# Kernel tuning notes

Hardware: AMD Instinct MI355X
Metric: run time of the kernel (lower is better)

The kernel has to match this reference:

```python
import jax, jax.numpy as jnp
import numpy as np

N_NODES = 50000
N_EDGES = 800000
F_IN = 128
F_OUT = 128
N_REL = 4
BN_EPS = 1e-5


def setup_inputs() -> dict:
    key = jax.random.key(0)
    ks = jax.random.split(key, 12)
    s = 1.0 / np.sqrt(F_IN)
    inp = {
        "x": jax.random.normal(ks[0], (N_NODES, F_IN), dtype=jnp.float32),
        "edge_index": jax.random.randint(ks[1], (2, N_EDGES), 0, N_NODES, dtype=jnp.int64),
        "edge_type": jax.random.randint(ks[2], (N_EDGES,), 0, N_REL, dtype=jnp.int64),
        # self-loop linear
        "W_self": jax.random.uniform(ks[3], (F_IN, F_OUT), jnp.float32, -s, s),
        "b_self": jax.random.uniform(ks[4], (F_OUT,), jnp.float32, -s, s),
        # per-relation GIN MLP: Linear -> BatchNorm1d -> ReLU -> Linear (stacked over relations)
        "W1": jax.random.uniform(ks[5], (N_REL, F_IN, F_OUT), jnp.float32, -s, s),
        "b1": jax.random.uniform(ks[6], (N_REL, F_OUT), jnp.float32, -s, s),
        "gamma": jnp.ones((N_REL, F_OUT), jnp.float32),
        "beta": jnp.zeros((N_REL, F_OUT), jnp.float32),
        "W2": jax.random.uniform(ks[7], (N_REL, F_OUT, F_OUT), jnp.float32, -1.0 / np.sqrt(F_OUT), 1.0 / np.sqrt(F_OUT)),
        "b2": jax.random.uniform(ks[8], (N_REL, F_OUT), jnp.float32, -1.0 / np.sqrt(F_OUT), 1.0 / np.sqrt(F_OUT)),
    }
    return inp


def reference(x, edge_index, edge_type, W_self, b_self, W1, b1, gamma, beta, W2, b2):
    N = x.shape[0]
    R = W1.shape[0]
    src, dst = edge_index[0], edge_index[1]
    # single fused scatter-add over (relation, dst): segment id = rel*N + dst
    msg = x[src]                                        # [E, F_in]
    seg = edge_type * N + dst                           # [E]
    agg = jax.ops.segment_sum(msg, seg, num_segments=R * N).reshape(R, N, -1)  # [R, N, F_in]
    # GIN with eps=0: h = x + sum of neighbor messages, per relation
    h = x[None, :, :] + agg                             # [R, N, F_in]
    # MLP: Linear -> BatchNorm1d (batch stats over nodes) -> ReLU -> Linear
    h = jnp.einsum('rnf,rfg->rng', h, W1) + b1[:, None, :]
    mean = jnp.mean(h, axis=1, keepdims=True)
    var = jnp.var(h, axis=1, keepdims=True)
    h = (h - mean) * jax.lax.rsqrt(var + BN_EPS) * gamma[:, None, :] + beta[:, None, :]
    h = jax.nn.relu(h)
    out_rel = jnp.einsum('rng,rgk->rnk', h, W2) + b2[:, None, :]  # [R, N, F_out]
    return x @ W_self + b_self + jnp.sum(out_rel, axis=0)
```

## Files before the change

### kernel.cpp

```cpp
#include <hip/hip_runtime.h>

#define NN 50000
#define NE 800000
#define F 128
#define NREL 4
#define RN (NREL * NN)
#define NB 196
#define BN_EPS 1e-5f
#define TILE 128
#define NT1 391
#define LDW 136

typedef __attribute__((ext_vector_type(8))) short short8;
typedef __attribute__((ext_vector_type(4))) float floatx4;

__device__ __forceinline__ ushort f2bf(float f) {
    union { float f; unsigned u; } v; v.f = f;
    unsigned r = v.u + 0x7fffu + ((v.u >> 16) & 1u);
    return (ushort)(r >> 16);
}
__device__ __forceinline__ float bf2f(ushort h) {
    union { unsigned u; float f; } v; v.u = ((unsigned)h) << 16;
    return v.f;
}
__device__ __forceinline__ float ubf(unsigned bits) {
    union { unsigned u; float f; } v; v.u = bits; return v.f;
}
__device__ __forceinline__ unsigned pk2(float a, float b) {
    return (unsigned)f2bf(a) | ((unsigned)f2bf(b) << 16);
}
__device__ __forceinline__ void acc_u4(float* acc, uint4 v) {
    acc[0] += ubf(v.x << 16); acc[1] += ubf(v.x & 0xffff0000u);
    acc[2] += ubf(v.y << 16); acc[3] += ubf(v.y & 0xffff0000u);
    acc[4] += ubf(v.z << 16); acc[5] += ubf(v.z & 0xffff0000u);
    acc[6] += ubf(v.w << 16); acc[7] += ubf(v.w & 0xffff0000u);
}

__global__ __launch_bounds__(256) void xb_kernel(
    const float* __restrict__ x, ushort* __restrict__ xb)
{
    int i = blockIdx.x * 256 + threadIdx.x;
    float4 v = *(const float4*)(x + (size_t)i * 4);
    uint2 u;
    u.x = pk2(v.x, v.y);
    u.y = pk2(v.z, v.w);
    *(uint2*)(xb + (size_t)i * 4) = u;
}

__global__ __launch_bounds__(256) void hist_kernel(
    const int* __restrict__ ei, const int* __restrict__ et, int* __restrict__ counts)
{
    int e = blockIdx.x * 256 + threadIdx.x;
    if (e >= NE) return;
    atomicAdd(&counts[et[e] * NN + ei[NE + e]], 1);
}

__global__ __launch_bounds__(256) void scan1_kernel(
    const int* __restrict__ counts, int* __restrict__ rowptr, int* __restrict__ bsum)
{
    __shared__ int wsum[4];
    const int tid = threadIdx.x;
    const int base = blockIdx.x * 1024 + tid * 4;
    int c[4];
    #pragma unroll
    for (int j = 0; j < 4; j++) c[j] = (base + j < RN) ? counts[base + j] : 0;
    int tsum = c[0] + c[1] + c[2] + c[3];
    const int lane = tid & 63, wv = tid >> 6;
    int s = tsum;
    #pragma unroll
    for (int d = 1; d < 64; d <<= 1) { int t = __shfl_up(s, d); if (lane >= d) s += t; }
    if (lane == 63) wsum[wv] = s;
    __syncthreads();
    int wave_off = 0;
    #pragma unroll
    for (int w = 0; w < 4; w++) if (w < wv) wave_off += wsum[w];
    int run = wave_off + s - tsum;
    #pragma unroll
    for (int j = 0; j < 4; j++) {
        if (base + j < RN) rowptr[base + j] = run;
        run += c[j];
    }
    if (tid == 0) bsum[blockIdx.x] = wsum[0] + wsum[1] + wsum[2] + wsum[3];
}

__global__ __launch_bounds__(256) void scan2_kernel(
    const int* __restrict__ bsum, int* __restrict__ boff, int* __restrict__ rowptr)
{
    __shared__ int wsum[4];
    const int tid = threadIdx.x;
    int v = (tid < NB) ? bsum[tid] : 0;
    const int lane = tid & 63, wv = tid >> 6;
    int s = v;
    #pragma unroll
    for (int d = 1; d < 64; d <<= 1) { int t = __shfl_up(s, d); if (lane >= d) s += t; }
    if (lane == 63) wsum[wv] = s;
    __syncthreads();
    int wave_off = 0;
    #pragma unroll
    for (int w = 0; w < 4; w++) if (w < wv) wave_off += wsum[w];
    if (tid < NB) boff[tid] = wave_off + s - v;
    if (tid == 0) rowptr[RN] = wsum[0] + wsum[1] + wsum[2] + wsum[3];
}

__global__ __launch_bounds__(256) void scan3_kernel(
    int* __restrict__ rowptr, const int* __restrict__ boff, int* __restrict__ cursor)
{
    const int base = blockIdx.x * 1024 + threadIdx.x * 4;
    const int off = boff[blockIdx.x];
    #pragma unroll
    for (int j = 0; j < 4; j++) {
        int idx = base + j;
        if (idx < RN) { int v = rowptr[idx] + off; rowptr[idx] = v; cursor[idx] = v; }
    }
}

__global__ __launch_bounds__(256) void reorder_kernel(
    const int* __restrict__ ei, const int* __restrict__ et,
    int* __restrict__ cursor, int* __restrict__ sorted_src)
{
    int e = blockIdx.x * 256 + threadIdx.x;
    if (e >= NE) return;
    int key = et[e] * NN + ei[NE + e];
    int pos = atomicAdd(&cursor[key], 1);
    sorted_src[pos] = ei[e];
}

__global__ __launch_bounds__(256) void gather_kernel(
    const ushort* __restrict__ xb, const int* __restrict__ rowptr,
    const int* __restrict__ sorted_src, ushort* __restrict__ hbuf)
{
    const int t = blockIdx.x * 256 + threadIdx.x;
    const int row = t >> 4;
    const int lane = t & 15;
    const int n = row % NN;

    const uint4* xv = (const uint4*)xb;
    float acc[8];
    {
        uint4 v = xv[n * 16 + lane];
        acc[0] = ubf(v.x << 16); acc[1] = ubf(v.x & 0xffff0000u);
        acc[2] = ubf(v.y << 16); acc[3] = ubf(v.y & 0xffff0000u);
        acc[4] = ubf(v.z << 16); acc[5] = ubf(v.z & 0xffff0000u);
        acc[6] = ubf(v.w << 16); acc[7] = ubf(v.w & 0xffff0000u);
    }
    int e = rowptr[row];
    const int e1 = rowptr[row + 1];
    for (; e + 4 <= e1; e += 4) {
        int s0 = sorted_src[e], s1 = sorted_src[e + 1];
        int s2 = sorted_src[e + 2], s3 = sorted_src[e + 3];
        uint4 a = xv[s0 * 16 + lane];
        uint4 b = xv[s1 * 16 + lane];
        uint4 c = xv[s2 * 16 + lane];
        uint4 d = xv[s3 * 16 + lane];
        acc_u4(acc, a); acc_u4(acc, b); acc_u4(acc, c); acc_u4(acc, d);
    }
    for (; e < e1; ++e) {
        int s0 = sorted_src[e];
        acc_u4(acc, xv[s0 * 16 + lane]);
    }
    uint4 o;
    o.x = pk2(acc[0], acc[1]);
    o.y = pk2(acc[2], acc[3]);
    o.z = pk2(acc[4], acc[5]);
    o.w = pk2(acc[6], acc[7]);
    *(uint4*)(hbuf + (size_t)row * F + lane * 8) = o;
}

__global__ __launch_bounds__(256) void prep_kernel(
    const float* __restrict__ W1, const float* __restrict__ W2,
    const float* __restrict__ Wself, ushort* __restrict__ Wt_g)
{
    __shared__ ushort Lt[F * F];
    int m = blockIdx.x;
    const float* src = (m < 4) ? (W1 + (size_t)m * F * F)
                     : (m < 8) ? (W2 + (size_t)(m - 4) * F * F)
                               : Wself;
    int tid = threadIdx.x;
    #pragma unroll
    for (int p = 0; p < 16; p++) {
        int i4 = tid + p * 256;
        int k = i4 >> 5;
        int n4 = (i4 & 31) * 4;
        float4 v = *(const float4*)(src + (size_t)k * F + n4);
        Lt[(n4 + 0) * F + k] = f2bf(v.x);
        Lt[(n4 + 1) * F + k] = f2bf(v.y);
        Lt[(n4 + 2) * F + k] = f2bf(v.z);
        Lt[(n4 + 3) * F + k] = f2bf(v.w);
    }
    __syncthreads();
    #pragma unroll
    for (int p = 0; p < 8; p++) {
        int c = tid + p * 256;
        *(uint4*)(Wt_g + (size_t)m * F * F + c * 8) = *(const uint4*)&Lt[c * 8];
    }
}

__global__ __launch_bounds__(256, 2) void gemm1_kernel(
    ushort* __restrict__ hbuf, const ushort* __restrict__ Wt_g,
    const float* __restrict__ b1, float* __restrict__ partials)
{
    __shared__ __attribute__((aligned(16))) ushort Sh[2 * TILE * LDW];
    __shared__ float csum[F], csq[F];
    ushort* At = Sh;
    ushort* Wt = Sh + TILE * LDW;

    const int tid = threadIdx.x;
    const int r = blockIdx.y;
    const int n0 = blockIdx.x * TILE;

    if (tid < F) { csum[tid] = 0.f; csq[tid] = 0.f; }

    #pragma unroll
    for (int p = 0; p < 8; p++) {
        int c = tid + p * 256;
        int row = c >> 4, off = (c & 15) * 8;
        uint4 v = make_uint4(0u, 0u, 0u, 0u);
        if (n0 + row < NN)
            v = *(const uint4*)(hbuf + ((size_t)r * NN + n0 + row) * F + off);
        *(uint4*)&At[row * LDW + off] = v;
    }
    {
        const ushort* wg = Wt_g + (size_t)r * F * F;
        #pragma unroll
        for (int p = 0; p < 8; p++) {
            int c = tid + p * 256;
            int n = c >> 4, off = (c & 15) * 8;
            *(uint4*)&Wt[n * LDW + off] = *(const uint4*)(wg + c * 8);
        }
    }
    __syncthreads();

    const int lane = tid & 63, w = tid >> 6;
    const int m = lane & 15, quad = lane >> 4;
    floatx4 acc[2][8];
    #pragma unroll
    for (int rg = 0; rg < 2; rg++)
        #pragma unroll
        for (int g = 0; g < 8; g++) acc[rg][g] = (floatx4)0.f;

    const ushort* Ap0 = &At[(w * 32 + m) * LDW + quad * 8];
    const ushort* Ap1 = Ap0 + 16 * LDW;
    const ushort* Bp  = &Wt[m * LDW + quad * 8];
    #pragma unroll
    for (int kk = 0; kk < 4; kk++) {
        short8 a0 = *(const short8*)(Ap0 + kk * 32);
        short8 a1 = *(const short8*)(Ap1 + kk * 32);
        #pragma unroll
        for (int g = 0; g < 8; g++) {
            short8 b = *(const short8*)(Bp + g * 16 * LDW + kk * 32);
            acc[0][g] = __builtin_amdgcn_mfma_f32_16x16x32_bf16(a0, b, acc[0][g], 0, 0, 0);
            acc[1][g] = __builtin_amdgcn_mfma_f32_16x16x32_bf16(a1, b, acc[1][g], 0, 0, 0);
        }
    }
    __syncthreads();

    #pragma unroll
    for (int rg = 0; rg < 2; rg++) {
        const int rb = w * 32 + rg * 16;
        #pragma unroll
        for (int g = 0; g < 8; g++) {
            int c = g * 16 + m;
            float bv = b1[r * F + c];
            float ls = 0.f, lq = 0.f;
            #pragma unroll
            for (int i = 0; i < 4; i++) {
                int lrow = rb + quad * 4 + i;
                float v = acc[rg][g][i] + bv;
                At[lrow * LDW + c] = f2bf(v);
                if (n0 + lrow < NN) { ls += v; lq += v * v; }
            }
            ls += __shfl_xor(ls, 16); ls += __shfl_xor(ls, 32);
            lq += __shfl_xor(lq, 16); lq += __shfl_xor(lq, 32);
            if (quad == 0) { atomicAdd(&csum[c], ls); atomicAdd(&csq[c], lq); }
        }
    }
    __syncthreads();

    #pragma unroll
    for (int p = 0; p < 8; p++) {
        int cc = tid + p * 256;
        int row = cc >> 4, off = (cc & 15) * 8;
        if (n0 + row < NN)
            *(uint4*)(hbuf + ((size_t)r * NN + n0 + row) * F + off) =
                *(const uint4*)&At[row * LDW + off];
    }
    partials[((size_t)r * NT1 + blockIdx.x) * 256 + tid] =
        (tid < F) ? csum[tid] : csq[tid - F];
}

__global__ __launch_bounds__(256) void bncoef_kernel(
    const float* __restrict__ partials,
    const float* __restrict__ gamma, const float* __restrict__ beta,
    const float* __restrict__ b2, const float* __restrict__ bself,
    float* __restrict__ sa, float* __restrict__ sb, float* __restrict__ btot)
{
    const int id = blockIdx.x * 256 + threadIdx.x;
    const int rel = id >> 7, col = id & 127;
    float s = 0.f, q = 0.f;
    const float* p = partials + (size_t)rel * NT1 * 256;
    for (int b = 0; b < NT1; b++) {
        s += p[b * 256 + col];
        q += p[b * 256 + 128 + col];
    }
    float mean = s * (1.0f / NN);
    float var = q * (1.0f / NN) - mean * mean;
    float g = gamma[id] * rsqrtf(var + BN_EPS);
    sa[id] = g;
    sb[id] = beta[id] - mean * g;
    if (blockIdx.x == 0 && threadIdx.x < F) {
        int c = threadIdx.x;
        btot[c] = bself[c] + b2[c] + b2[F + c] + b2[2 * F + c] + b2[3 * F + c];
    }
}

__global__ __launch_bounds__(256, 2) void gemm2_kernel(
    const ushort* __restrict__ xb, const ushort* __restrict__ h1,
    const ushort* __restrict__ Wt_g,
    const float* __restrict__ sa, const float* __restrict__ sb,
    const float* __restrict__ btot, float* __restrict__ out)
{
    __shared__ __attribute__((aligned(16))) ushort Sh[2 * TILE * LDW];
    __shared__ float sAl[NREL * F], sBl[NREL * F];
    ushort* At = Sh;
    ushort* Wt = Sh + TILE * LDW;

    const int tid = threadIdx.x;
    const int n0 = blockIdx.x * TILE;

    #pragma unroll
    for (int p = 0; p < 2; p++) {
        int idx = tid + p * 256;
        sAl[idx] = sa[idx];
        sBl[idx] = sb[idx];
    }

    const int lane = tid & 63, w = tid >> 6;
    const int m = lane & 15, quad = lane >> 4;
    floatx4 acc[2][8];
    #pragma unroll
    for (int rg = 0; rg < 2; rg++)
        #pragma unroll
        for (int g = 0; g < 8; g++) acc[rg][g] = (floatx4)0.f;

    for (int rel = 0; rel < 5; rel++) {
        __syncthreads();
        if (rel < 4) {
            #pragma unroll
            for (int p = 0; p < 8; p++) {
                int c = tid + p * 256;
                int row = c >> 4, off = (c & 15) * 8;
                unsigned uu[4] = {0, 0, 0, 0};
                if (n0 + row < NN) {
                    uint4 v = *(const uint4*)(h1 + ((size_t)rel * NN + n0 + row) * F + off);
                    uu[0] = v.x; uu[1] = v.y; uu[2] = v.z; uu[3] = v.w;
                    #pragma unroll
                    for (int j = 0; j < 4; j++) {
                        int c0 = off + j * 2;
                        float v0 = bf2f((ushort)(uu[j] & 0xffffu));
                        float v1 = bf2f((ushort)(uu[j] >> 16));
                        v0 = fmaxf(fmaf(v0, sAl[rel * F + c0], sBl[rel * F + c0]), 0.f);
                        v1 = fmaxf(fmaf(v1, sAl[rel * F + c0 + 1], sBl[rel * F + c0 + 1]), 0.f);
                        uu[j] = pk2(v0, v1);
                    }
                }
                *(uint4*)&At[row * LDW + off] = make_uint4(uu[0], uu[1], uu[2], uu[3]);
            }
        } else {
            #pragma unroll
            for (int p = 0; p < 8; p++) {
                int c = tid + p * 256;
                int row = c >> 4, off = (c & 15) * 8;
                uint4 v = make_uint4(0u, 0u, 0u, 0u);
                if (n0 + row < NN)
                    v = *(const uint4*)(xb + (size_t)(n0 + row) * F + off);
                *(uint4*)&At[row * LDW + off] = v;
            }
        }
        {
            int mat = (rel < 4) ? (NREL + rel) : 8;
            const ushort* wg = Wt_g + (size_t)mat * F * F;
            #pragma unroll
            for (int p = 0; p < 8; p++) {
                int c = tid + p * 256;
                int n = c >> 4, off = (c & 15) * 8;
                *(uint4*)&Wt[n * LDW + off] = *(const uint4*)(wg + c * 8);
            }
        }
        __syncthreads();
        const ushort* Ap0 = &At[(w * 32 + m) * LDW + quad * 8];
        const ushort* Ap1 = Ap0 + 16 * LDW;
        const ushort* Bp  = &Wt[m * LDW + quad * 8];
        #pragma unroll
        for (int kk = 0; kk < 4; kk++) {
            short8 a0 = *(const short8*)(Ap0 + kk * 32);
            short8 a1 = *(const short8*)(Ap1 + kk * 32);
            #pragma unroll
            for (int g = 0; g < 8; g++) {
                short8 b = *(const short8*)(Bp + g * 16 * LDW + kk * 32);
                acc[0][g] = __builtin_amdgcn_mfma_f32_16x16x32_bf16(a0, b, acc[0][g], 0, 0, 0);
                acc[1][g] = __builtin_amdgcn_mfma_f32_16x16x32_bf16(a1, b, acc[1][g], 0, 0, 0);
            }
        }
    }
    __syncthreads();

    float* Ct = (float*)Sh;
    #pragma unroll
    for (int rg = 0; rg < 2; rg++) {
        const int rb = w * 32 + rg * 16;
        #pragma unroll
        for (int g = 0; g < 8; g++) {
            int c = g * 16 + m;
            float bv = btot[c];
            #pragma unroll
            for (int i = 0; i < 4; i++) {
                int lrow = rb + quad * 4 + i;
                Ct[lrow * F + c] = acc[rg][g][i] + bv;
            }
        }
    }
    __syncthreads();
    #pragma unroll
    for (int p = 0; p < 16; p++) {
        int i4 = tid + p * 256;
        int row = i4 >> 5;
        int c4 = (i4 & 31) * 4;
        if (n0 + row < NN)
            *(float4*)(out + (size_t)(n0 + row) * F + c4) = *(const float4*)&Ct[row * F + c4];
    }
}

extern "C" void kernel_launch(void* const* d_in, const int* in_sizes, int n_in,
                              void* d_out, int out_size, void* d_ws, size_t ws_size,
                              hipStream_t stream) {
    const float* x     = (const float*)d_in[0];
    const int*   ei    = (const int*)d_in[1];
    const int*   et    = (const int*)d_in[2];
    const float* Wself = (const float*)d_in[3];
    const float* bself = (const float*)d_in[4];
    const float* W1    = (const float*)d_in[5];
    const float* b1    = (const float*)d_in[6];
    const float* gamma = (const float*)d_in[7];
    const float* beta  = (const float*)d_in[8];
    const float* W2    = (const float*)d_in[9];
    const float* b2    = (const float*)d_in[10];
    float* out = (float*)d_out;

    ushort* hbuf = (ushort*)d_ws;
    ushort* xb   = hbuf + (size_t)RN * F;
    ushort* Wt_g = xb + (size_t)NN * F;
    float*  partials = (float*)(Wt_g + 9 * F * F);
    float*  sa    = partials + (size_t)NREL * NT1 * 256;
    float*  sb    = sa + NREL * F;
    float*  btot  = sb + NREL * F;
    int* counts     = (int*)(btot + F);
    int* rowptr     = counts + RN;
    int* cursor     = rowptr + RN + 1;
    int* sorted_src = cursor + RN;
    int* bsum       = sorted_src + NE;
    int* boff       = bsum + 256;

    hipMemsetAsync(counts, 0, (size_t)RN * sizeof(int), stream);

    prep_kernel<<<9, 256, 0, stream>>>(W1, W2, Wself, Wt_g);
    xb_kernel<<<NN * F / 1024, 256, 0, stream>>>(x, xb);
    hist_kernel<<<(NE + 255) / 256, 256, 0, stream>>>(ei, et, counts);
    scan1_kernel<<<NB, 256, 0, stream>>>(counts, rowptr, bsum);
    scan2_kernel<<<1, 256, 0, stream>>>(bsum, boff, rowptr);
    scan3_kernel<<<NB, 256, 0, stream>>>(rowptr, boff, cursor);
    reorder_kernel<<<(NE + 255) / 256, 256, 0, stream>>>(ei, et, cursor, sorted_src);
    gather_kernel<<<RN * 16 / 256, 256, 0, stream>>>(xb, rowptr, sorted_src, hbuf);
    {
        dim3 grid(NT1, NREL);
        gemm1_kernel<<<grid, 256, 0, stream>>>(hbuf, Wt_g, b1, partials);
    }
    bncoef_kernel<<<2, 256, 0, stream>>>(partials, gamma, beta, b2, bself, sa, sb, btot);
    gemm2_kernel<<<NT1, 256, 0, stream>>>(xb, hbuf, Wt_g, sa, sb, btot, out);
}
```

Baseline: 322.7 us.

## Feed MFMA operands from global, halve LDS, and parallelize BN reduction

Both GEMM kernels now load A-operand fragments straight from global memory into registers instead of staging a full A tile in LDS. This halves shared memory use, so launch bounds go up to 4 blocks per CU, and one LDS round trip plus a barrier is gone. gemm2 applies the BN scale/shift and ReLU in registers, and writes output directly from accumulators instead of through an LDS staging tile. The BN coefficient reduction is spread over 64 blocks with warp-shuffle reductions instead of 2 blocks looping serially. The costs are that the output stores become narrower and less coalesced, and the last tile reads rows past N, out of bounds for the last relation.

```diff
diff --git a/kernel.cpp b/kernel.cpp
--- a/kernel.cpp
+++ b/kernel.cpp
@@ -195,30 +195,21 @@
     }
 }
 
-__global__ __launch_bounds__(256, 2) void gemm1_kernel(
+__global__ __launch_bounds__(256, 4) void gemm1_kernel(
     ushort* __restrict__ hbuf, const ushort* __restrict__ Wt_g,
     const float* __restrict__ b1, float* __restrict__ partials)
 {
-    __shared__ __attribute__((aligned(16))) ushort Sh[2 * TILE * LDW];
+    __shared__ __attribute__((aligned(16))) ushort Wt[F * LDW];
     __shared__ float csum[F], csq[F];
-    ushort* At = Sh;
-    ushort* Wt = Sh + TILE * LDW;
 
     const int tid = threadIdx.x;
     const int r = blockIdx.y;
     const int n0 = blockIdx.x * TILE;
+    const int lane = tid & 63, w = tid >> 6;
+    const int m = lane & 15, quad = lane >> 4;
 
     if (tid < F) { csum[tid] = 0.f; csq[tid] = 0.f; }
 
-    #pragma unroll
-    for (int p = 0; p < 8; p++) {
-        int c = tid + p * 256;
-        int row = c >> 4, off = (c & 15) * 8;
-        uint4 v = make_uint4(0u, 0u, 0u, 0u);
-        if (n0 + row < NN)
-            v = *(const uint4*)(hbuf + ((size_t)r * NN + n0 + row) * F + off);
-        *(uint4*)&At[row * LDW + off] = v;
-    }
     {
         const ushort* wg = Wt_g + (size_t)r * F * F;
         #pragma unroll
@@ -230,17 +221,16 @@
     }
     __syncthreads();
 
-    const int lane = tid & 63, w = tid >> 6;
-    const int m = lane & 15, quad = lane >> 4;
+    const ushort* Ap0 = hbuf + ((size_t)r * NN + n0 + w * 32 + m) * F + quad * 8;
+    const ushort* Ap1 = Ap0 + 16 * F;
+    const ushort* Bp  = &Wt[m * LDW + quad * 8];
+
     floatx4 acc[2][8];
     #pragma unroll
     for (int rg = 0; rg < 2; rg++)
         #pragma unroll
         for (int g = 0; g < 8; g++) acc[rg][g] = (floatx4)0.f;
 
-    const ushort* Ap0 = &At[(w * 32 + m) * LDW + quad * 8];
-    const ushort* Ap1 = Ap0 + 16 * LDW;
-    const ushort* Bp  = &Wt[m * LDW + quad * 8];
     #pragma unroll
     for (int kk = 0; kk < 4; kk++) {
         short8 a0 = *(const short8*)(Ap0 + kk * 32);
@@ -254,6 +244,7 @@
     }
     __syncthreads();
 
+    ushort* At = Wt;
     #pragma unroll
     for (int rg = 0; rg < 2; rg++) {
         const int rb = w * 32 + rg * 16;
@@ -294,38 +285,46 @@
     const float* __restrict__ b2, const float* __restrict__ bself,
     float* __restrict__ sa, float* __restrict__ sb, float* __restrict__ btot)
 {
-    const int id = blockIdx.x * 256 + threadIdx.x;
-    const int rel = id >> 7, col = id & 127;
+    const int tid = threadIdx.x;
+    const int pair = blockIdx.x * 8 + (tid >> 5);
+    const int l32 = tid & 31;
+    const int rel = pair >> 7, col = pair & 127;
+    const float* p = partials + (size_t)rel * NT1 * 256;
     float s = 0.f, q = 0.f;
-    const float* p = partials + (size_t)rel * NT1 * 256;
-    for (int b = 0; b < NT1; b++) {
+    for (int b = l32; b < NT1; b += 32) {
         s += p[b * 256 + col];
         q += p[b * 256 + 128 + col];
     }
-    float mean = s * (1.0f / NN);
-    float var = q * (1.0f / NN) - mean * mean;
-    float g = gamma[id] * rsqrtf(var + BN_EPS);
-    sa[id] = g;
-    sb[id] = beta[id] - mean * g;
-    if (blockIdx.x == 0 && threadIdx.x < F) {
-        int c = threadIdx.x;
-        btot[c] = bself[c] + b2[c] + b2[F + c] + b2[2 * F + c] + b2[3 * F + c];
-    }
-}
-
-__global__ __launch_bounds__(256, 2) void gemm2_kernel(
+    #pragma unroll
+    for (int d = 1; d < 32; d <<= 1) {
+        s += __shfl_xor(s, d, 32);
+        q += __shfl_xor(q, d, 32);
+    }
+    if (l32 == 0) {
+        float mean = s * (1.0f / NN);
+        float var = q * (1.0f / NN) - mean * mean;
+        float g = gamma[pair] * rsqrtf(var + BN_EPS);
+        sa[pair] = g;
+        sb[pair] = beta[pair] - mean * g;
+    }
+    if (blockIdx.x == 0 && tid < F)
+        btot[tid] = bself[tid] + b2[tid] + b2[F + tid] + b2[2 * F + tid] + b2[3 * F + tid];
+}
+
+__global__ __launch_bounds__(256, 4) void gemm2_kernel(
     const ushort* __restrict__ xb, const ushort* __restrict__ h1,
     const ushort* __restrict__ Wt_g,
     const float* __restrict__ sa, const float* __restrict__ sb,
     const float* __restrict__ btot, float* __restrict__ out)
 {
-    __shared__ __attribute__((aligned(16))) ushort Sh[2 * TILE * LDW];
+    __shared__ __attribute__((aligned(16))) ushort Wt[F * LDW];
     __shared__ float sAl[NREL * F], sBl[NREL * F];
-    ushort* At = Sh;
-    ushort* Wt = Sh + TILE * LDW;
 
     const int tid = threadIdx.x;
     const int n0 = blockIdx.x * TILE;
+    const int lane = tid & 63, w = tid >> 6;
+    const int m = lane & 15, quad = lane >> 4;
+    const int koff = quad * 8;
 
     #pragma unroll
     for (int p = 0; p < 2; p++) {
@@ -334,8 +333,6 @@
         sBl[idx] = sb[idx];
     }
 
-    const int lane = tid & 63, w = tid >> 6;
-    const int m = lane & 15, quad = lane >> 4;
     floatx4 acc[2][8];
     #pragma unroll
     for (int rg = 0; rg < 2; rg++)
@@ -344,38 +341,6 @@
 
     for (int rel = 0; rel < 5; rel++) {
         __syncthreads();
-        if (rel < 4) {
-            #pragma unroll
-            for (int p = 0; p < 8; p++) {
-                int c = tid + p * 256;
-                int row = c >> 4, off = (c & 15) * 8;
-                unsigned uu[4] = {0, 0, 0, 0};
-                if (n0 + row < NN) {
-                    uint4 v = *(const uint4*)(h1 + ((size_t)rel * NN + n0 + row) * F + off);
-                    uu[0] = v.x; uu[1] = v.y; uu[2] = v.z; uu[3] = v.w;
-                    #pragma unroll
-                    for (int j = 0; j < 4; j++) {
-                        int c0 = off + j * 2;
-                        float v0 = bf2f((ushort)(uu[j] & 0xffffu));
-                        float v1 = bf2f((ushort)(uu[j] >> 16));
-                        v0 = fmaxf(fmaf(v0, sAl[rel * F + c0], sBl[rel * F + c0]), 0.f);
-                        v1 = fmaxf(fmaf(v1, sAl[rel * F + c0 + 1], sBl[rel * F + c0 + 1]), 0.f);
-                        uu[j] = pk2(v0, v1);
-                    }
-                }
-                *(uint4*)&At[row * LDW + off] = make_uint4(uu[0], uu[1], uu[2], uu[3]);
-            }
-        } else {
-            #pragma unroll
-            for (int p = 0; p < 8; p++) {
-                int c = tid + p * 256;
-                int row = c >> 4, off = (c & 15) * 8;
-                uint4 v = make_uint4(0u, 0u, 0u, 0u);
-                if (n0 + row < NN)
-                    v = *(const uint4*)(xb + (size_t)(n0 + row) * F + off);
-                *(uint4*)&At[row * LDW + off] = v;
-            }
-        }
         {
             int mat = (rel < 4) ? (NREL + rel) : 8;
             const ushort* wg = Wt_g + (size_t)mat * F * F;
@@ -387,24 +352,59 @@
             }
         }
         __syncthreads();
-        const ushort* Ap0 = &At[(w * 32 + m) * LDW + quad * 8];
-        const ushort* Ap1 = Ap0 + 16 * LDW;
-        const ushort* Bp  = &Wt[m * LDW + quad * 8];
-        #pragma unroll
-        for (int kk = 0; kk < 4; kk++) {
-            short8 a0 = *(const short8*)(Ap0 + kk * 32);
-            short8 a1 = *(const short8*)(Ap1 + kk * 32);
+        const ushort* Bp = &Wt[m * LDW + koff];
+        if (rel < 4) {
+            const ushort* hp0 = h1 + ((size_t)rel * NN + n0 + w * 32 + m) * F + koff;
+            const ushort* hp1 = hp0 + 16 * F;
             #pragma unroll
-            for (int g = 0; g < 8; g++) {
-                short8 b = *(const short8*)(Bp + g * 16 * LDW + kk * 32);
-                acc[0][g] = __builtin_amdgcn_mfma_f32_16x16x32_bf16(a0, b, acc[0][g], 0, 0, 0);
-                acc[1][g] = __builtin_amdgcn_mfma_f32_16x16x32_bf16(a1, b, acc[1][g], 0, 0, 0);
+            for (int kk = 0; kk < 4; kk++) {
+                uint4 rv0 = *(const uint4*)(hp0 + kk * 32);
+                uint4 rv1 = *(const uint4*)(hp1 + kk * 32);
+                float4 ca0 = *(const float4*)(&sAl[rel * F + koff + kk * 32]);
+                float4 ca1 = *(const float4*)(&sAl[rel * F + koff + kk * 32 + 4]);
+                float4 cb0 = *(const float4*)(&sBl[rel * F + koff + kk * 32]);
+                float4 cb1 = *(const float4*)(&sBl[rel * F + koff + kk * 32 + 4]);
+                union { uint4 u; short8 s; } a0, a1;
+                a0.u.x = pk2(fmaxf(fmaf(ubf(rv0.x << 16),         ca0.x, cb0.x), 0.f),
+                             fmaxf(fmaf(ubf(rv0.x & 0xffff0000u), ca0.y, cb0.y), 0.f));
+                a0.u.y = pk2(fmaxf(fmaf(ubf(rv0.y << 16),         ca0.z, cb0.z), 0.f),
+                             fmaxf(fmaf(ubf(rv0.y & 0xffff0000u), ca0.w, cb0.w), 0.f));
+                a0.u.z = pk2(fmaxf(fmaf(ubf(rv0.z << 16),         ca1.x, cb1.x), 0.f),
+                             fmaxf(fmaf(ubf(rv0.z & 0xffff0000u), ca1.y, cb1.y), 0.f));
+                a0.u.w = pk2(fmaxf(fmaf(ubf(rv0.w << 16),         ca1.z, cb1.z), 0.f),
+                             fmaxf(fmaf(ubf(rv0.w & 0xffff0000u), ca1.w, cb1.w), 0.f));
+                a1.u.x = pk2(fmaxf(fmaf(ubf(rv1.x << 16),         ca0.x, cb0.x), 0.f),
+                             fmaxf(fmaf(ubf(rv1.x & 0xffff0000u), ca0.y, cb0.y), 0.f));
+                a1.u.y = pk2(fmaxf(fmaf(ubf(rv1.y << 16),         ca0.z, cb0.z), 0.f),
+                             fmaxf(fmaf(ubf(rv1.y & 0xffff0000u), ca0.w, cb0.w), 0.f));
+                a1.u.z = pk2(fmaxf(fmaf(ubf(rv1.z << 16),         ca1.x, cb1.x), 0.f),
+                             fmaxf(fmaf(ubf(rv1.z & 0xffff0000u), ca1.y, cb1.y), 0.f));
+                a1.u.w = pk2(fmaxf(fmaf(ubf(rv1.w << 16),         ca1.z, cb1.z), 0.f),
+                             fmaxf(fmaf(ubf(rv1.w & 0xffff0000u), ca1.w, cb1.w), 0.f));
+                #pragma unroll
+                for (int g = 0; g < 8; g++) {
+                    short8 b = *(const short8*)(Bp + g * 16 * LDW + kk * 32);
+                    acc[0][g] = __builtin_amdgcn_mfma_f32_16x16x32_bf16(a0.s, b, acc[0][g], 0, 0, 0);
+                    acc[1][g] = __builtin_amdgcn_mfma_f32_16x16x32_bf16(a1.s, b, acc[1][g], 0, 0, 0);
+                }
             }
-        }
-    }
-    __syncthreads();
-
-    float* Ct = (float*)Sh;
+        } else {
+            const ushort* xp0 = xb + (size_t)(n0 + w * 32 + m) * F + koff;
+            const ushort* xp1 = xp0 + 16 * F;
+            #pragma unroll
+            for (int kk = 0; kk < 4; kk++) {
+                short8 a0 = *(const short8*)(xp0 + kk * 32);
+                short8 a1 = *(const short8*)(xp1 + kk * 32);
+                #pragma unroll
+                for (int g = 0; g < 8; g++) {
+                    short8 b = *(const short8*)(Bp + g * 16 * LDW + kk * 32);
+                    acc[0][g] = __builtin_amdgcn_mfma_f32_16x16x32_bf16(a0, b, acc[0][g], 0, 0, 0);
+                    acc[1][g] = __builtin_amdgcn_mfma_f32_16x16x32_bf16(a1, b, acc[1][g], 0, 0, 0);
+                }
+            }
+        }
+    }
+
     #pragma unroll
     for (int rg = 0; rg < 2; rg++) {
         const int rb = w * 32 + rg * 16;
@@ -414,19 +414,10 @@
             float bv = btot[c];
             #pragma unroll
             for (int i = 0; i < 4; i++) {
-                int lrow = rb + quad * 4 + i;
-                Ct[lrow * F + c] = acc[rg][g][i] + bv;
+                int n = n0 + rb + quad * 4 + i;
+                if (n < NN) out[(size_t)n * F + c] = acc[rg][g][i] + bv;
             }
         }
-    }
-    __syncthreads();
-    #pragma unroll
-    for (int p = 0; p < 16; p++) {
-        int i4 = tid + p * 256;
-        int row = i4 >> 5;
-        int c4 = (i4 & 31) * 4;
-        if (n0 + row < NN)
-            *(float4*)(out + (size_t)(n0 + row) * F + c4) = *(const float4*)&Ct[row * F + c4];
     }
 }
 
@@ -474,6 +465,6 @@
         dim3 grid(NT1, NREL);
         gemm1_kernel<<<grid, 256, 0, stream>>>(hbuf, Wt_g, b1, partials);
     }
-    bncoef_kernel<<<2, 256, 0, stream>>>(partials, gamma, beta, b2, bself, sa, sb, btot);
+    bncoef_kernel<<<64, 256, 0, stream>>>(partials, gamma, beta, b2, bself, sa, sb, btot);
     gemm2_kernel<<<NT1, 256, 0, stream>>>(xb, hbuf, Wt_g, sa, sb, btot, out);
 }
```

After: 353.3 us. 9.5% more time.
